# Optimization experiments

Hardware: AMD Instinct MI355X
Metric: run time of the kernel (lower is better)

The kernel has to match this reference:

```python
import jax, jax.numpy as jnp
import numpy as np

BN_EPS = 1e-3  # keras BatchNormalization default epsilon; moving_mean=0, moving_var=1 (init values, inference mode)

def _bn(x, gamma, beta):
    # inference BN with mean=0, var=1: gamma*(x)/sqrt(1+eps) + beta, broadcast over last (channel) axis
    return x * (gamma / jnp.sqrt(1.0 + BN_EPS)) + beta

def _rel_embed(rel, K):
    # reproduces: concat_i rel[K-1-i : 2K-1-i, :] along axis=1 -> emb[a, i] = rel[a - i + K - 1]
    idx = jnp.arange(K)[:, None] - jnp.arange(K)[None, :] + (K - 1)  # [K, K]
    return rel[idx, 0, :]  # [K, K, c]

def _forward(x, w_q, w_k, w_v, q_rel, k_rel, v_rel,
             g_q, b_q, g_k, b_k, g_v, b_v, g_qk, b_qk, g_qr, b_qr,
             g_kr, b_kr, g_sv, b_sv, g_sve, b_sve):
    N, H, W, C = x.shape
    G = g_qk.shape[0]                 # groups = 8
    out_ch = w_v.shape[1]             # 128
    gc = out_ch // G                  # group_ch = 16
    K = H                             # kernel_size == H

    # 1x1 conv transforms (no bias) + BN
    q = _bn(jnp.einsum('bhwc,cd->bhwd', x, w_q), g_q, b_q)  # [N,H,W,out/2]
    k = _bn(jnp.einsum('bhwc,cd->bhwd', x, w_k), g_k, b_k)  # [N,H,W,out/2]
    v = _bn(jnp.einsum('bhwc,cd->bhwd', x, w_v), g_v, b_v)  # [N,H,W,out]

    q_emb = _rel_embed(q_rel, K)  # [K,K,gc/2], used with subscript 'ijc'
    k_emb = _rel_embed(k_rel, K)
    v_emb = _rel_embed(v_rel, K)  # [K,K,gc], used with subscript 'jic'

    q5 = q.reshape(N, H, W, G, gc // 2)
    k5 = k.reshape(N, H, W, G, gc // 2)
    v5 = v.reshape(N, H, W, G, gc)

    qr = jnp.einsum('biwgc,ijc->bijwg', q5, q_emb)   # [N,H,H,W,G]
    qr = _bn(qr, g_qr, b_qr)                         # BN over groups (last axis), same as on (N,-1,W,G)
    kr = jnp.einsum('biwgc,ijc->bijwg', k5, k_emb)
    kr = _bn(kr, g_kr, b_kr)
    kr = jnp.transpose(kr, (0, 2, 1, 3, 4))          # swap i<->j as in source

    qk = jnp.einsum('biwgc,bjwgc->bijwg', q5, k5)    # [N,H,H,W,G]
    qk = _bn(qk, g_qk, b_qk)

    # NOTE: faithful to source: softmax over axis=-2 (the W axis of bijwg)
    sim = jax.nn.softmax(qk + qr + kr, axis=-2)

    sv = jnp.einsum('bijwg,bjwgc->biwgc', sim, v5)   # [N,H,W,G,gc]
    sve = jnp.einsum('bijwg,jic->biwgc', sim, v_emb)

    out = _bn(sv.reshape(N, H, W, out_ch), g_sv, b_sv) + _bn(sve.reshape(N, H, W, out_ch), g_sve, b_sve)
    return out  # [N,H,W,out_ch]


def setup_inputs() -> dict:
    key = jax.random.key(0)
    ks = jax.random.split(key, 32)
    N, H, W, C = 32, 56, 56, 128
    OUT, G, K = 128, 8, 56
    gc = OUT // G  # 16

    x = jax.random.normal(ks[0], (N, H, W, C), jnp.float32)

    w_q = jax.random.normal(ks[1], (C, OUT // 2), jnp.float32) * np.sqrt(1.0 / C * gc)
    w_k = jax.random.normal(ks[2], (C, OUT // 2), jnp.float32) * np.sqrt(1.0 / C)
    w_v = jax.random.normal(ks[3], (C, OUT), jnp.float32) * np.sqrt(1.0 / C)

    q_rel = jax.random.normal(ks[4], (2 * K - 1, 1, gc // 2), jnp.float32) * np.sqrt(1.0 / (OUT // 2))
    k_rel = jax.random.normal(ks[5], (2 * K - 1, 1, gc // 2), jnp.float32) * np.sqrt(1.0 / (OUT // 2))
    v_rel = jax.random.normal(ks[6], (2 * K - 1, 1, gc), jnp.float32) * np.sqrt(1.0 / OUT)

    def bn_params(k1, k2, c):
        gamma = jax.random.uniform(k1, (c,), jnp.float32, 0.5, 1.5)
        beta = 0.1 * jax.random.normal(k2, (c,), jnp.float32)
        return gamma, beta

    g_q, b_q = bn_params(ks[7], ks[8], OUT // 2)
    g_k, b_k = bn_params(ks[9], ks[10], OUT // 2)
    g_v, b_v = bn_params(ks[11], ks[12], OUT)
    g_qk, b_qk = bn_params(ks[13], ks[14], G)
    g_qr, b_qr = bn_params(ks[15], ks[16], G)
    g_kr, b_kr = bn_params(ks[17], ks[18], G)
    g_sv, b_sv = bn_params(ks[19], ks[20], OUT)
    g_sve, b_sve = bn_params(ks[21], ks[22], OUT)

    return dict(x=x, w_q=w_q, w_k=w_k, w_v=w_v, q_rel=q_rel, k_rel=k_rel, v_rel=v_rel,
                g_q=g_q, b_q=b_q, g_k=g_k, b_k=b_k, g_v=g_v, b_v=b_v,
                g_qk=g_qk, b_qk=b_qk, g_qr=g_qr, b_qr=b_qr, g_kr=g_kr, b_kr=b_kr,
                g_sv=g_sv, b_sv=b_sv, g_sve=g_sve, b_sve=b_sve)


def reference(x, w_q, w_k, w_v, q_rel, k_rel, v_rel,
              g_q, b_q, g_k, b_k, g_v, b_v, g_qk, b_qk, g_qr, b_qr,
              g_kr, b_kr, g_sv, b_sv, g_sve, b_sve):
    return _forward(x, w_q, w_k, w_v, q_rel, k_rel, v_rel,
                    g_q, b_q, g_k, b_k, g_v, b_v, g_qk, b_qk, g_qr, b_qr,
                    g_kr, b_kr, g_sv, b_sv, g_sve, b_sve)
```

## Files before the change

### kernel.cpp

```cpp
#include <hip/hip_runtime.h>
#include <math.h>


typedef _Float16 f16;
typedef _Float16 f16x2 __attribute__((ext_vector_type(2)));
typedef _Float16 f16x4 __attribute__((ext_vector_type(4)));
typedef _Float16 f16x8 __attribute__((ext_vector_type(8)));
typedef float    f32x4 __attribute__((ext_vector_type(4)));
typedef unsigned int u32;
typedef unsigned int u32x2 __attribute__((ext_vector_type(2)));

static constexpr int NB    = 32;
static constexpr int HH    = 56;
static constexpr int CIN   = 128;
static constexpr int GG    = 8;
static constexpr int PLANE = HH * HH;
static constexpr int MT    = 112;
static constexpr int NBLK  = 28;

__global__ __launch_bounds__(256) void prep_kernel(
    const float* __restrict__ wq, const float* __restrict__ wk,
    const float* __restrict__ wv, f16* __restrict__ wt)
{
    const int id = blockIdx.x * 256 + threadIdx.x;
    const int d = id >> 4, kc = id & 15;
    const float* src; int stride, dl;
    if (d < 64)       { src = wq; stride = 64;  dl = d; }
    else if (d < 128) { src = wk; stride = 64;  dl = d - 64; }
    else              { src = wv; stride = 128; dl = d - 128; }
    f16x8 v;
    #pragma unroll
    for (int kk = 0; kk < 8; ++kk)
        v[kk] = (f16)src[(kc * 8 + kk) * stride + dl];
    *(f16x8*)&wt[d * 128 + kc * 8] = v;
}

__global__ __launch_bounds__(256, 2) void qkv_kernel(
    const float* __restrict__ x, const f16* __restrict__ wt,
    const float* __restrict__ gq, const float* __restrict__ bq,
    const float* __restrict__ gk, const float* __restrict__ bk,
    const float* __restrict__ gv, const float* __restrict__ bv,
    f16* __restrict__ qt, f16* __restrict__ kt, f16* __restrict__ vt2)
{
    __shared__ f16 lds_a[MT * 136];
    __shared__ f16 lds_b[128 * 136];

    const int t    = threadIdx.x;
    const int nh   = blockIdx.y;
    const int b    = blockIdx.x / NBLK;
    const int B28  = blockIdx.x - b * NBLK;
    const int rem0 = B28 * MT;
    const size_t m0 = (size_t)b * PLANE + rem0;

    {
        const float4* xs = (const float4*)(x + m0 * CIN);
        #pragma unroll
        for (int it = 0; it < 14; ++it) {
            const int f = it * 256 + t;
            const int r = f >> 5, c = f & 31;
            const float4 v = xs[f];
            f16x4 p; p.x = (f16)v.x; p.y = (f16)v.y; p.z = (f16)v.z; p.w = (f16)v.w;
            *(f16x4*)&lds_a[r * 136 + c * 4] = p;
        }
    }
    #pragma unroll
    for (int it = 0; it < 8; ++it) {
        const int f = it * 256 + t;
        const int n = f >> 4, kc = f & 15;
        *(f16x8*)&lds_b[n * 136 + kc * 8] =
            *(const f16x8*)&wt[(size_t)(nh * 128 + n) * 128 + kc * 8];
    }
    __syncthreads();

    const int lane = t & 63, wid = t >> 6;
    const int wn0 = wid * 32;
    const int ra = lane & 15, qd = lane >> 4;

    f32x4 acc[7][2];
    #pragma unroll
    for (int mt = 0; mt < 7; ++mt)
        #pragma unroll
        for (int nt = 0; nt < 2; ++nt)
            acc[mt][nt] = (f32x4){0.f, 0.f, 0.f, 0.f};

    #pragma unroll
    for (int ks = 0; ks < 4; ++ks) {
        f16x8 af[7], bf[2];
        #pragma unroll
        for (int mt = 0; mt < 7; ++mt)
            af[mt] = *(const f16x8*)&lds_a[(mt * 16 + ra) * 136 + ks * 32 + qd * 8];
        #pragma unroll
        for (int nt = 0; nt < 2; ++nt)
            bf[nt] = *(const f16x8*)&lds_b[(wn0 + nt * 16 + ra) * 136 + ks * 32 + qd * 8];
        #pragma unroll
        for (int mt = 0; mt < 7; ++mt)
            #pragma unroll
            for (int nt = 0; nt < 2; ++nt)
                acc[mt][nt] = __builtin_amdgcn_mfma_f32_16x16x32_f16(
                    af[mt], bf[nt], acc[mt][nt], 0, 0, 0);
    }
    __syncthreads();

    f16* lds_c = lds_a;
    const float inv = 1.0f / sqrtf(1.001f);
    #pragma unroll
    for (int nt = 0; nt < 2; ++nt) {
        const int d  = wn0 + nt * 16 + ra;
        const int dg = nh * 128 + d;
        float scale, shift;
        if (dg < 64)       { scale = gq[dg] * inv;        shift = bq[dg]; }
        else if (dg < 128) { scale = gk[dg - 64] * inv;   shift = bk[dg - 64]; }
        else               { scale = gv[dg - 128] * inv;  shift = bv[dg - 128]; }
        #pragma unroll
        for (int mt = 0; mt < 7; ++mt)
            #pragma unroll
            for (int rg = 0; rg < 4; ++rg) {
                const int m = mt * 16 + qd * 4 + rg;
                lds_c[m * 136 + d] = (f16)fmaf(acc[mt][nt][rg], scale, shift);
            }
    }
    __syncthreads();

    if (nh == 0) {
        const int rl = t & 31, gs2 = t >> 5;
        #pragma unroll
        for (int it = 0; it < 4; ++it) {
            const int rem = it * 32 + rl;
            if (rem < MT) {
                #pragma unroll
                for (int half = 0; half < 2; ++half) {
                    const int gslot = half * 8 + gs2;
                    const f16x8 v = *(const f16x8*)&lds_c[rem * 136 + gslot * 8];
                    f16* dst = (gslot < 8) ? qt : kt;
                    const int g = gslot & 7;
                    *(f16x8*)&dst[((size_t)(b * GG + g) * PLANE + rem0 + rem) * 8] = v;
                }
            }
        }
    } else {
        const int cq = t & 3, w8 = (t >> 2) & 7, g = t >> 5;
        #pragma unroll
        for (int it = 0; it < 7; ++it) {
            const int w = it * 8 + w8;
            const int doff = g * 16 + cq * 4;
            const u32x2 a  = *(const u32x2*)&lds_c[w * 136 + doff];
            const u32x2 bb = *(const u32x2*)&lds_c[(56 + w) * 136 + doff];
            uint4 o;
            o.x = __builtin_amdgcn_perm(a.x, bb.x, 0x01000504u);
            o.y = __builtin_amdgcn_perm(a.x, bb.x, 0x03020706u);
            o.z = __builtin_amdgcn_perm(a.y, bb.y, 0x01000504u);
            o.w = __builtin_amdgcn_perm(a.y, bb.y, 0x03020706u);
            const size_t base =
                (((size_t)(b * GG + g) * NBLK + B28) * HH + w) * 32 + cq * 8;
            *(uint4*)&vt2[base] = o;
        }
    }
}

__global__ __launch_bounds__(256) void attn_kernel(
    const f16* __restrict__ qt, const f16* __restrict__ kt, const f16* __restrict__ vt2,
    const float* __restrict__ q_rel, const float* __restrict__ k_rel, const float* __restrict__ v_rel,
    const float* __restrict__ g_qk, const float* __restrict__ b_qk,
    const float* __restrict__ g_qr, const float* __restrict__ b_qr,
    const float* __restrict__ g_kr, const float* __restrict__ b_kr,
    const float* __restrict__ g_sv, const float* __restrict__ b_sv,
    const float* __restrict__ g_sve, const float* __restrict__ b_sve,
    float* __restrict__ out)
{
    const int i = blockIdx.x;
    const int g = blockIdx.y;
    const int b = blockIdx.z;
    const int t = threadIdx.x;

    __shared__ f16 qi[56 * 8];
    __shared__ f16 qe[56 * 8];
    __shared__ f16 ke[56 * 8];
    __shared__ f16 ve2[28 * 32];
    __shared__ f16 s16[56 * 58];

    const float inv = 1.0f / sqrtf(1.001f);
    const int bg = (b * GG + g) * PLANE;

    if (t < 56)
        *(f16x8*)&qi[t * 8] = *(const f16x8*)&qt[(size_t)(bg + i * HH + t) * 8];
    for (int idx = t; idx < 448; idx += 256) {
        const int j = idx >> 3, c = idx & 7;
        qe[idx] = (f16)q_rel[(i - j + 55) * 8 + c];
        ke[idx] = (f16)k_rel[(j - i + 55) * 8 + c];
    }
    for (int idx = t; idx < 896; idx += 256) {
        const int J = idx >> 5, r = idx & 31, c = r >> 1, jb = r & 1;
        ve2[idx] = (f16)v_rel[(2 * J + jb - i + 55) * 16 + c];
    }
    const float sqk = g_qk[g] * inv, bqk = b_qk[g];
    const float sqr = g_qr[g] * inv, bqr = b_qr[g];
    const float skr = g_kr[g] * inv, bkr = b_kr[g];
    __syncthreads();

    {
        const int wv = t >> 6, lane = t & 63;
        const int wc = (lane < 56) ? lane : 55;
        const f16x8 qv = *(const f16x8*)&qi[wc * 8];
        for (int jj = 0; jj < 14; ++jj) {
            const int j = wv * 14 + jj;
            const f16x8 kv = *(const f16x8*)&kt[(size_t)(bg + j * HH + wc) * 8];
            const f16x8 ev = *(const f16x8*)&qe[j * 8];
            const f16x8 fv = *(const f16x8*)&ke[j * 8];
            float qk = 0.f, qr = 0.f, kr = 0.f;
            #pragma unroll
            for (int c = 0; c < 4; ++c) {
                const f16x2 kk = ((const f16x2*)&kv)[c];
                const f16x2 qq = ((const f16x2*)&qv)[c];
                qk = __builtin_amdgcn_fdot2(qq, kk, qk, false);
                qr = __builtin_amdgcn_fdot2(qq, ((const f16x2*)&ev)[c], qr, false);
                kr = __builtin_amdgcn_fdot2(kk, ((const f16x2*)&fv)[c], kr, false);
            }
            const float s = fmaf(sqk, qk, bqk) + fmaf(sqr, qr, bqr) + fmaf(skr, kr, bkr);
            float mx = (lane < 56) ? s : -3.0e38f;
            #pragma unroll
            for (int off = 1; off <= 32; off <<= 1)
                mx = fmaxf(mx, __shfl_xor(mx, off));
            float e = (lane < 56) ? __expf(s - mx) : 0.f;
            float sum = e;
            #pragma unroll
            for (int off = 1; off <= 32; off <<= 1)
                sum += __shfl_xor(sum, off);
            const float p = e * __builtin_amdgcn_rcpf(sum);
            if (lane < 56) s16[lane * 58 + j] = (f16)p;
        }
    }
    __syncthreads();

    if (t < 224) {
        const int w = t >> 2, cq = t & 3;
        const f16* vp = vt2 + ((size_t)(b * GG + g) * NBLK * HH + w) * 32 + cq * 8;
        float sv[4] = {0.f, 0.f, 0.f, 0.f};
        float se[4] = {0.f, 0.f, 0.f, 0.f};
        #pragma unroll 4
        for (int J = 0; J < 28; ++J) {
            const f16x2 pp = *(const f16x2*)&s16[w * 58 + 2 * J];
            const f16x8 vl = *(const f16x8*)(vp + (size_t)J * (HH * 32));
            const f16x8 el = *(const f16x8*)&ve2[J * 32 + cq * 8];
            #pragma unroll
            for (int c = 0; c < 4; ++c) {
                sv[c] = __builtin_amdgcn_fdot2(pp, ((const f16x2*)&vl)[c], sv[c], false);
                se[c] = __builtin_amdgcn_fdot2(pp, ((const f16x2*)&el)[c], se[c], false);
            }
        }
        const int ch = g * 16 + cq * 4;
        const float4 gsv  = *(const float4*)(g_sv + ch);
        const float4 bsv  = *(const float4*)(b_sv + ch);
        const float4 gsve = *(const float4*)(g_sve + ch);
        const float4 bsve = *(const float4*)(b_sve + ch);
        float4 o;
        o.x = fmaf(gsv.x * inv, sv[0], bsv.x) + fmaf(gsve.x * inv, se[0], bsve.x);
        o.y = fmaf(gsv.y * inv, sv[1], bsv.y) + fmaf(gsve.y * inv, se[1], bsve.y);
        o.z = fmaf(gsv.z * inv, sv[2], bsv.z) + fmaf(gsve.z * inv, se[2], bsve.z);
        o.w = fmaf(gsv.w * inv, sv[3], bsv.w) + fmaf(gsve.w * inv, se[3], bsve.w);
        *(float4*)(out + ((size_t)(b * HH + i) * HH + w) * 128 + ch) = o;
    }
}

extern "C" void kernel_launch(void* const* d_in, const int* in_sizes, int n_in,
                              void* d_out, int out_size, void* d_ws, size_t ws_size,
                              hipStream_t stream)
{
    const float* x     = (const float*)d_in[0];
    const float* w_q   = (const float*)d_in[1];
    const float* w_k   = (const float*)d_in[2];
    const float* w_v   = (const float*)d_in[3];
    const float* q_rel = (const float*)d_in[4];
    const float* k_rel = (const float*)d_in[5];
    const float* v_rel = (const float*)d_in[6];
    const float* g_q   = (const float*)d_in[7];
    const float* b_q   = (const float*)d_in[8];
    const float* g_k   = (const float*)d_in[9];
    const float* b_k   = (const float*)d_in[10];
    const float* g_v   = (const float*)d_in[11];
    const float* b_v   = (const float*)d_in[12];
    const float* g_qk  = (const float*)d_in[13];
    const float* b_qk  = (const float*)d_in[14];
    const float* g_qr  = (const float*)d_in[15];
    const float* b_qr  = (const float*)d_in[16];
    const float* g_kr  = (const float*)d_in[17];
    const float* b_kr  = (const float*)d_in[18];
    const float* g_sv  = (const float*)d_in[19];
    const float* b_sv  = (const float*)d_in[20];
    const float* g_sve = (const float*)d_in[21];
    const float* b_sve = (const float*)d_in[22];
    float* out = (float*)d_out;

    f16* wt  = (f16*)d_ws;
    f16* qt  = wt + 32768;
    f16* kt  = qt + (size_t)NB * GG * PLANE * 8;
    f16* vt2 = kt + (size_t)NB * GG * PLANE * 8;

    prep_kernel<<<16, 256, 0, stream>>>(w_q, w_k, w_v, wt);

    qkv_kernel<<<dim3((NB * PLANE) / MT, 2), 256, 0, stream>>>(
        x, wt, g_q, b_q, g_k, b_k, g_v, b_v, qt, kt, vt2);

    attn_kernel<<<dim3(56, 8, 32), 256, 0, stream>>>(
        qt, kt, vt2, q_rel, k_rel, v_rel,
        g_qk, b_qk, g_qr, b_qr, g_kr, b_kr, g_sv, b_sv, g_sve, b_sve, out);
}
```

Baseline: 304.4 us.

## Move softmax out of per-row wave reductions into a separate shared-memory pass

Logits are written to an fp32 shared buffer instead of being softmaxed immediately with 12 cross-lane shuffles per (j) row. A new pass has 4 threads per row each handle 14 elements serially, then combine with two shuffles per reduction before writing fp16 probabilities. This cuts shuffle and exp-serialisation overhead but adds a barrier and about 12.7KB of extra LDS, which may lower occupancy. The sv loop now reads probability pairs as f16x4 with adjusted unrolling. The f16x4 load at offset w*58+2J may be only 4-byte aligned for odd w.

Measured after the change: 254.5 us. 1.2x faster.

```diff
diff --git a/kernel.cpp b/kernel.cpp
--- a/kernel.cpp
+++ b/kernel.cpp
@@ -172,11 +172,12 @@
     const int b = blockIdx.z;
     const int t = threadIdx.x;
 
+    __shared__ float s32[56][57];
+    __shared__ f16 s16[56 * 58];
     __shared__ f16 qi[56 * 8];
     __shared__ f16 qe[56 * 8];
     __shared__ f16 ke[56 * 8];
     __shared__ f16 ve2[28 * 32];
-    __shared__ f16 s16[56 * 58];
 
     const float inv = 1.0f / sqrtf(1.001f);
     const int bg = (b * GG + g) * PLANE;
@@ -216,18 +217,32 @@
                 kr = __builtin_amdgcn_fdot2(kk, ((const f16x2*)&fv)[c], kr, false);
             }
             const float s = fmaf(sqk, qk, bqk) + fmaf(sqr, qr, bqr) + fmaf(skr, kr, bkr);
-            float mx = (lane < 56) ? s : -3.0e38f;
-            #pragma unroll
-            for (int off = 1; off <= 32; off <<= 1)
-                mx = fmaxf(mx, __shfl_xor(mx, off));
-            float e = (lane < 56) ? __expf(s - mx) : 0.f;
-            float sum = e;
-            #pragma unroll
-            for (int off = 1; off <= 32; off <<= 1)
-                sum += __shfl_xor(sum, off);
-            const float p = e * __builtin_amdgcn_rcpf(sum);
-            if (lane < 56) s16[lane * 58 + j] = (f16)p;
-        }
+            if (lane < 56) s32[j][lane] = s;
+        }
+    }
+    __syncthreads();
+
+    if (t < 224) {
+        const int j = t >> 2, q = t & 3;
+        const int w0 = q * 14;
+        float v[14];
+        #pragma unroll
+        for (int wi = 0; wi < 14; ++wi) v[wi] = s32[j][w0 + wi];
+        float mx = v[0];
+        #pragma unroll
+        for (int wi = 1; wi < 14; ++wi) mx = fmaxf(mx, v[wi]);
+        mx = fmaxf(mx, __shfl_xor(mx, 1));
+        mx = fmaxf(mx, __shfl_xor(mx, 2));
+        float e[14];
+        float sum = 0.f;
+        #pragma unroll
+        for (int wi = 0; wi < 14; ++wi) { e[wi] = __expf(v[wi] - mx); sum += e[wi]; }
+        sum += __shfl_xor(sum, 1);
+        sum += __shfl_xor(sum, 2);
+        const float rs = __builtin_amdgcn_rcpf(sum);
+        #pragma unroll
+        for (int wi = 0; wi < 14; ++wi)
+            s16[(w0 + wi) * 58 + j] = (f16)(e[wi] * rs);
     }
     __syncthreads();
 
@@ -236,15 +251,19 @@
         const f16* vp = vt2 + ((size_t)(b * GG + g) * NBLK * HH + w) * 32 + cq * 8;
         float sv[4] = {0.f, 0.f, 0.f, 0.f};
         float se[4] = {0.f, 0.f, 0.f, 0.f};
-        #pragma unroll 4
-        for (int J = 0; J < 28; ++J) {
-            const f16x2 pp = *(const f16x2*)&s16[w * 58 + 2 * J];
-            const f16x8 vl = *(const f16x8*)(vp + (size_t)J * (HH * 32));
-            const f16x8 el = *(const f16x8*)&ve2[J * 32 + cq * 8];
+        #pragma unroll 2
+        for (int J = 0; J < 28; J += 2) {
+            const f16x4 pp4 = *(const f16x4*)&s16[w * 58 + 2 * J];
             #pragma unroll
-            for (int c = 0; c < 4; ++c) {
-                sv[c] = __builtin_amdgcn_fdot2(pp, ((const f16x2*)&vl)[c], sv[c], false);
-                se[c] = __builtin_amdgcn_fdot2(pp, ((const f16x2*)&el)[c], se[c], false);
+            for (int u = 0; u < 2; ++u) {
+                const f16x2 pp = ((const f16x2*)&pp4)[u];
+                const f16x8 vl = *(const f16x8*)(vp + (size_t)(J + u) * (HH * 32));
+                const f16x8 el = *(const f16x8*)&ve2[(J + u) * 32 + cq * 8];
+                #pragma unroll
+                for (int c = 0; c < 4; ++c) {
+                    sv[c] = __builtin_amdgcn_fdot2(pp, ((const f16x2*)&vl)[c], sv[c], false);
+                    se[c] = __builtin_amdgcn_fdot2(pp, ((const f16x2*)&el)[c], se[c], false);
+                }
             }
         }
         const int ch = g * 16 + cq * 4;
```
